# Kernel optimization log

Measured on AMD Instinct MI355X. Metric: run time of the kernel, lower is better.

Reference implementation:

```python
import jax, jax.numpy as jnp
import numpy as np

B, T, S, A = 4, 10, 6, 6
HID, L, IMG = 512, 6, 128
NCH = 16  # spatial-softmax channels
_px, _py = np.meshgrid(np.linspace(-1.0, 1.0, IMG), np.linspace(-1.0, 1.0, IMG))
POSX = jnp.asarray(_px.reshape(-1), jnp.float32)
POSY = jnp.asarray(_py.reshape(-1), jnp.float32)


def _conv_relu(x, w, b):
    y = jax.lax.conv_general_dilated(x, w, (1, 1), 'SAME',
                                     dimension_numbers=('NCHW', 'OIHW', 'NCHW'))
    return jax.nn.relu(y + b[None, :, None, None])


def _cnn_ss(x, ws, bs):
    for w, b in zip(ws, bs):
        x = _conv_relu(x, w, b)
    n = x.shape[0]
    attn = jax.nn.softmax(x.reshape(n, NCH, -1), axis=-1)  # (n, 16, H*W)
    ex = attn @ POSX  # (n, 16)
    ey = attn @ POSY
    return jnp.stack([ex, ey], axis=-1).reshape(n, 2 * NCH)  # (n, 32)


def _lstm_cell(x, h, c, wih, whh, bih, bhh):
    g = x @ wih.T + bih + h @ whh.T + bhh
    i, f, gg, o = jnp.split(g, 4, axis=-1)  # torch LSTMCell gate order i,f,g,o
    c2 = jax.nn.sigmoid(f) * c + jax.nn.sigmoid(i) * jnp.tanh(gg)
    h2 = jax.nn.sigmoid(o) * jnp.tanh(c2)
    return h2, c2


def setup_inputs() -> dict:
    key = jax.random.key(0)
    ks = iter(jax.random.split(key, 64))

    def nrm(shape, s=0.05):
        return jax.random.normal(next(ks), shape, dtype=jnp.float32) * s

    inp = {
        'seq_img_main': nrm((B, T, 3, IMG, IMG), 1.0),
        'seq_img_secondary': nrm((B, T, 3, IMG, IMG), 1.0),
        'seq_states': nrm((B, T, S), 1.0),
    }
    chans = [(32, 3), (64, 32), (128, 64), (16, 128)]
    for cam in ('m', 's'):
        for j, (o, ci) in enumerate(chans):
            inp[f'{cam}_w{j}'] = nrm((o, ci, 3, 3))
            inp[f'{cam}_b{j}'] = nrm((o,))
    in0, inr = S + 64, HID + 64  # 70 and 576
    inp['wih0'] = nrm((4 * HID, in0)); inp['whh0'] = nrm((4 * HID, HID))
    inp['bih0'] = nrm((4 * HID,)); inp['bhh0'] = nrm((4 * HID,))
    inp['wih_r'] = nrm((L - 1, 4 * HID, inr)); inp['whh_r'] = nrm((L - 1, 4 * HID, HID))
    inp['bih_r'] = nrm((L - 1, 4 * HID)); inp['bhh_r'] = nrm((L - 1, 4 * HID))
    inp['out_w'] = nrm((A, inr)); inp['out_b'] = nrm((A,))
    return inp


def reference(seq_img_main, seq_img_secondary, seq_states,
              m_w0, m_b0, m_w1, m_b1, m_w2, m_b2, m_w3, m_b3,
              s_w0, s_b0, s_w1, s_b1, s_w2, s_b2, s_w3, s_b3,
              wih0, whh0, bih0, bhh0, wih_r, whh_r, bih_r, bhh_r,
              out_w, out_b):
    b, t = seq_img_main.shape[:2]
    fm = _cnn_ss(seq_img_main.reshape(b * t, 3, IMG, IMG),
                 [m_w0, m_w1, m_w2, m_w3], [m_b0, m_b1, m_b2, m_b3])
    fs = _cnn_ss(seq_img_secondary.reshape(b * t, 3, IMG, IMG),
                 [s_w0, s_w1, s_w2, s_w3], [s_b0, s_b1, s_b2, s_b3])
    img = jnp.concatenate([fm, fs], axis=-1).reshape(b, t, 64)  # (B,T,64)

    h0 = jnp.zeros((L, b, HID), jnp.float32)
    c0 = jnp.zeros((L, b, HID), jnp.float32)

    def step(carry, xt):
        h, c = carry
        st, im = xt  # (B,S), (B,64)
        x = jnp.concatenate([st, im], axis=-1)
        hn, cn = _lstm_cell(x, h[0], c[0], wih0, whh0, bih0, bhh0)
        hs, cs = [hn], [cn]
        for l in range(L - 1):
            x = jnp.concatenate([hs[-1], im], axis=-1)
            hl, cl = _lstm_cell(x, h[l + 1], c[l + 1],
                                wih_r[l], whh_r[l], bih_r[l], bhh_r[l])
            hs.append(hl); cs.append(cl)
        out = jnp.concatenate([hs[-1], im], axis=-1) @ out_w.T + out_b
        return (jnp.stack(hs), jnp.stack(cs)), out

    _, outs = jax.lax.scan(step, (h0, c0),
                           (seq_states.transpose(1, 0, 2), img.transpose(1, 0, 2)))
    return outs.transpose(1, 0, 2)  # (B,T,A)
```

## Files before the change

### kernel.cpp

```cpp
#include <hip/hip_runtime.h>
#include <hip/hip_bf16.h>
#include <math.h>

typedef __hip_bfloat16 bf16;
typedef short bf16x8 __attribute__((ext_vector_type(8)));
typedef float f32x4 __attribute__((ext_vector_type(4)));

static constexpr int HWPX = 16384;

__device__ inline float sigmoidf_(float x) { return 1.0f / (1.0f + expf(-x)); }
__device__ inline float bflo(unsigned u) { return __uint_as_float(u << 16); }
__device__ inline float bfhi(unsigned u) { return __uint_as_float(u & 0xffff0000u); }
__device__ inline int swz(int x) { return (x ^ (x >> 2)) & 3; }

__device__ inline void gll16(const bf16* g, short* l) {
    __builtin_amdgcn_global_load_lds(
        (const __attribute__((address_space(1))) void*)g,
        (__attribute__((address_space(3))) void*)l, 16, 0, 0);
}

__global__ __launch_bounds__(256) void prep_lstm_k(
    const float* __restrict__ wih0, const float* __restrict__ whh0,
    const float* __restrict__ wihr, const float* __restrict__ whhr,
    bf16* __restrict__ d0, bf16* __restrict__ d1,
    bf16* __restrict__ d2, bf16* __restrict__ d3)
{
    const size_t nA = 2048ull * 72, nB = 2048ull * 512;
    const size_t nC = 5ull * 2048 * 576, nD = 5ull * 2048 * 512;
    for (size_t i = blockIdx.x * 256ull + threadIdx.x; i < nA + nB + nC + nD;
         i += (size_t)gridDim.x * 256) {
        if (i < nA) {
            int c = (int)(i % 72), r = (int)(i / 72);
            d0[i] = __float2bfloat16(c < 70 ? wih0[(size_t)r * 70 + c] : 0.f);
        } else if (i < nA + nB) {
            size_t k = i - nA; d1[k] = __float2bfloat16(whh0[k]);
        } else if (i < nA + nB + nC) {
            size_t k = i - nA - nB; d2[k] = __float2bfloat16(wihr[k]);
        } else {
            size_t k = i - nA - nB - nC; d3[k] = __float2bfloat16(whhr[k]);
        }
    }
}

struct ConvW {
    const float* src[8];
    bf16* dst[8];
};

__global__ __launch_bounds__(256) void prep_conv_k(ConvW a)
{
    const int sizes[4] = {3072, 18432, 73728, 18432};
    const int cins[4] = {3, 32, 64, 128};
    const int couts[4] = {32, 64, 128, 16};
    int total = 2 * 113664;
    for (int idx = blockIdx.x * 256 + threadIdx.x; idx < total; idx += gridDim.x * 256) {
        int i = idx, cam = 0;
        if (i >= 113664) { cam = 1; i -= 113664; }
        int layer = 0;
        while (layer < 3 && i >= sizes[layer]) { i -= sizes[layer]; ++layer; }
        const float* w = a.src[cam * 4 + layer];
        bf16* d = a.dst[cam * 4 + layer];
        if (layer == 0) {
            int k = i & 31, co = (i >> 5) & 31, ky = i >> 10;
            int kx = k >> 3, c = k & 7;
            float v = (kx < 3 && c < 3) ? w[((co * 3 + c) * 3 + ky) * 3 + kx] : 0.f;
            d[i] = __float2bfloat16(v);
        } else {
            int CIN = cins[layer], COUT = couts[layer], KC = CIN / 32;
            int e = i & 7;
            int t2 = i >> 3;
            int co = t2 % COUT;
            int t3 = t2 / COUT;
            int q = t3 & 3;
            int t4 = t3 >> 2;
            int kc = t4 % KC;
            int tap = t4 / KC;
            d[i] = __float2bfloat16(w[((size_t)(co * CIN + kc * 32 + q * 8 + e)) * 9 + tap]);
        }
    }
}

__global__ __launch_bounds__(256, 4) void conv01(
    const float* __restrict__ srcm, const float* __restrict__ srcs,
    const bf16* __restrict__ w0m, const bf16* __restrict__ w0s,
    const float* __restrict__ b0m, const float* __restrict__ b0s,
    const bf16* __restrict__ wTm, const bf16* __restrict__ wTs,
    const float* __restrict__ bm, const float* __restrict__ bs,
    bf16* __restrict__ out, int c0)
{
    constexpr int COUT = 64, MW = 2;
    constexpr int SLOTS = 4 * 264;

    const int y0 = (blockIdx.x >> 1) * 2;
    const int x0 = (blockIdx.x & 1) * 64;
    const int cam = blockIdx.y;
    const int img = blockIdx.z;
    const int ci_ = cam * gridDim.z + img;
    const float* inImg = (cam ? srcs : srcm) + (size_t)(c0 + img) * 3 * HWPX;
    const bf16* wT0 = cam ? w0s : w0m;
    const float* bias0 = cam ? b0s : b0m;
    const bf16* wT = cam ? wTs : wTm;
    const float* bias = cam ? bs : bm;
    const int tid = threadIdx.x;
    const int wave = tid >> 6, lane = tid & 63;
    const int wrow = wave >> 1, wm = wave & 1;
    const int q = lane >> 4, n16 = lane & 15;

    __shared__ short smem[SLOTS * 8];
    __shared__ short raw[6 * 68 * 16];

    for (int i = tid; i < SLOTS; i += 256)
        *(bf16x8*)(void*)&smem[i * 8] = (bf16x8)0;

    for (int d = tid; d < 6 * 68; d += 256) {
        int x = d % 68, r = d / 68;
        int yy = y0 - 2 + r, xx = x0 - 2 + x;
        bf16 v8[8];
#pragma unroll
        for (int c = 0; c < 8; ++c) v8[c] = __float2bfloat16(0.f);
        if ((unsigned)yy < 128u && (unsigned)xx < 128u) {
            int o = yy * 128 + xx;
            v8[0] = __float2bfloat16(inImg[o]);
            v8[1] = __float2bfloat16(inImg[HWPX + o]);
            v8[2] = __float2bfloat16(inImg[2 * HWPX + o]);
        }
        *(bf16x8*)(void*)&raw[d * 16] = *(bf16x8*)(void*)v8;
        *(bf16x8*)(void*)&raw[d * 16 + 8] = (bf16x8)0;
    }
    __syncthreads();

    const int co0_ = wm * 16 + n16;
    for (int rp = 0; rp < 4; ++rp) {
        int Y = y0 - 1 + rp;
        if ((unsigned)Y >= 128u) continue;
        for (int xg = wrow; xg < 5; xg += 2) {
            int xt = xg * 16 + n16;
            int xts = xt < 66 ? xt : 65;
            f32x4 a0 = f32x4{0.f, 0.f, 0.f, 0.f};
#pragma unroll
            for (int ky = 0; ky < 3; ++ky) {
                bf16x8 aF = *(const bf16x8*)(const void*)(wT0 +
                    ((size_t)(ky * 32 + co0_) * 32) + q * 8);
                int off = (q < 3) ? ((rp + ky) * 68 + xts + q) * 16
                                  : ((rp + ky) * 68 + xts) * 16 + 8;
                bf16x8 bF = *(const bf16x8*)(const void*)&raw[off];
                a0 = __builtin_amdgcn_mfma_f32_16x16x32_bf16(aF, bF, a0, 0, 0, 0);
            }
            int X = x0 - 1 + xt;
            if (xt < 66 && (unsigned)X < 128u) {
                int cb0 = wm * 16 + q * 4;
                bf16 tmp[4];
#pragma unroll
                for (int r = 0; r < 4; ++r) {
                    float v = a0[r] + bias0[cb0 + r];
                    tmp[r] = __float2bfloat16(v > 0.f ? v : 0.f);
                }
                int g = cb0 >> 3;
                int sbase = (rp * 264 + xt * 4 + (g ^ swz(xt))) * 8 + (q & 1) * 4;
                *reinterpret_cast<uint2*>(&smem[sbase]) = *reinterpret_cast<uint2*>(tmp);
            }
        }
    }
    __syncthreads();

    f32x4 acc[MW][4];
#pragma unroll
    for (int mt = 0; mt < MW; ++mt)
#pragma unroll
        for (int nt = 0; nt < 4; ++nt) acc[mt][nt] = f32x4{0.f, 0.f, 0.f, 0.f};

#pragma unroll
    for (int ky = 0; ky < 3; ++ky) {
#pragma unroll
        for (int kx = 0; kx < 3; ++kx) {
            bf16x8 aF[MW];
#pragma unroll
            for (int mt = 0; mt < MW; ++mt) {
                int co = (wm * MW + mt) * 16 + n16;
                aF[mt] = *(const bf16x8*)(const void*)(wT +
                    (((size_t)(ky * 3 + kx) * 4 + q) * COUT + co) * 8);
            }
#pragma unroll
            for (int nt = 0; nt < 4; ++nt) {
                int xt = nt * 16 + n16 + kx;
                int slot = (wrow + ky) * 264 + xt * 4 + (q ^ swz(xt));
                bf16x8 bF = *(const bf16x8*)(const void*)&smem[slot * 8];
#pragma unroll
                for (int mt = 0; mt < MW; ++mt)
                    acc[mt][nt] = __builtin_amdgcn_mfma_f32_16x16x32_bf16(
                        aF[mt], bF, acc[mt][nt], 0, 0, 0);
            }
        }
    }

    const int y = y0 + wrow;
#pragma unroll
    for (int mt = 0; mt < MW; ++mt) {
        int co0 = (wm * MW + mt) * 16 + q * 4;
#pragma unroll
        for (int nt = 0; nt < 4; ++nt) {
            int x = x0 + nt * 16 + n16;
            bf16 tmp[4];
#pragma unroll
            for (int r = 0; r < 4; ++r) {
                float v = acc[mt][nt][r] + bias[co0 + r];
                tmp[r] = __float2bfloat16(v > 0.f ? v : 0.f);
            }
            *reinterpret_cast<uint2*>(out + ((size_t)ci_ * HWPX + y * 128 + x) * COUT + co0)
                = *reinterpret_cast<uint2*>(tmp);
        }
    }
}

template <int CIN, int COUT>
__global__ __launch_bounds__(256, 4) void conv2r(
    const bf16* __restrict__ in, const bf16* __restrict__ wTm,
    const bf16* __restrict__ wTs, const float* __restrict__ bm,
    const float* __restrict__ bs, bf16* __restrict__ out,
    const char* __restrict__ zpage)
{
    constexpr int KC = CIN / 32;
    constexpr int NB = (KC > 1) ? 2 : 1;
    constexpr int MW = COUT / 32;
    constexpr int SLOTS = 4 * 264;

    const int y0 = (blockIdx.x >> 1) * 2;
    const int x0 = (blockIdx.x & 1) * 64;
    const int cam = blockIdx.y;
    const int img = blockIdx.z;
    const int ci_ = cam * gridDim.z + img;
    const bf16* wT = cam ? wTs : wTm;
    const float* bias = cam ? bs : bm;
    const int tid = threadIdx.x;
    const int wave = tid >> 6, lane = tid & 63;
    const int wrow = wave >> 1, wm = wave & 1;
    const int q = lane >> 4, n16 = lane & 15;

    __shared__ short smem[NB][SLOTS * 8];
    const bf16* inImg = in + (size_t)ci_ * HWPX * CIN;

    const bf16* sptr[5];
#pragma unroll
    for (int it = 0; it < 5; ++it) {
        int s = it * 256 + tid;
        int r = s / 264, s2 = s - r * 264;
        int sx = s2 >> 2;
        int g = (s2 & 3) ^ swz(sx);
        int yy = y0 + r - 1, xx = x0 + sx - 1;
        bool ok = (s < SLOTS) && ((unsigned)yy < 128u) && ((unsigned)xx < 128u);
        sptr[it] = ok ? inImg + ((size_t)yy * 128 + xx) * CIN + g * 8
                      : (const bf16*)(zpage + (tid & 255) * 16);
    }
    auto stage = [&](int kc, int buf) {
#pragma unroll
        for (int it = 0; it < 5; ++it) {
            if (it * 256 + tid < SLOTS)
                gll16(sptr[it] + kc * 32, &smem[buf][it * 2048 + wave * 512]);
        }
    };

    f32x4 acc[MW][4];
#pragma unroll
    for (int mt = 0; mt < MW; ++mt)
#pragma unroll
        for (int nt = 0; nt < 4; ++nt) acc[mt][nt] = f32x4{0.f, 0.f, 0.f, 0.f};

    stage(0, 0);
    for (int kc = 0; kc < KC; ++kc) {
        __syncthreads();
        if (kc + 1 < KC) stage(kc + 1, (kc + 1) % NB);
        const short* sb = smem[kc % NB];
#pragma unroll
        for (int ky = 0; ky < 3; ++ky) {
#pragma unroll
            for (int kx = 0; kx < 3; ++kx) {
                bf16x8 aF[MW];
#pragma unroll
                for (int mt = 0; mt < MW; ++mt) {
                    int co = (wm * MW + mt) * 16 + n16;
                    aF[mt] = *(const bf16x8*)(const void*)(wT +
                        ((((size_t)(ky * 3 + kx) * KC + kc) * 4 + q) * COUT + co) * 8);
                }
#pragma unroll
                for (int nt = 0; nt < 4; ++nt) {
                    int xt = nt * 16 + n16 + kx;
                    int slot = (wrow + ky) * 264 + xt * 4 + (q ^ swz(xt));
                    bf16x8 bF = *(const bf16x8*)(const void*)&sb[slot * 8];
#pragma unroll
                    for (int mt = 0; mt < MW; ++mt)
                        acc[mt][nt] = __builtin_amdgcn_mfma_f32_16x16x32_bf16(
                            aF[mt], bF, acc[mt][nt], 0, 0, 0);
                }
            }
        }
    }

    const int y = y0 + wrow;
#pragma unroll
    for (int mt = 0; mt < MW; ++mt) {
        int co0 = (wm * MW + mt) * 16 + q * 4;
#pragma unroll
        for (int nt = 0; nt < 4; ++nt) {
            int x = x0 + nt * 16 + n16;
            bf16 tmp[4];
#pragma unroll
            for (int r = 0; r < 4; ++r) {
                float v = acc[mt][nt][r] + bias[co0 + r];
                tmp[r] = __float2bfloat16(v > 0.f ? v : 0.f);
            }
            *reinterpret_cast<uint2*>(out + ((size_t)ci_ * HWPX + y * 128 + x) * COUT + co0)
                = *reinterpret_cast<uint2*>(tmp);
        }
    }
}

__global__ __launch_bounds__(256, 6) void conv4_xs(
    const bf16* __restrict__ in, const bf16* __restrict__ wTm,
    const bf16* __restrict__ wTs, const float* __restrict__ bm,
    const float* __restrict__ bs,
    float* __restrict__ partial,
    const char* __restrict__ zpage, int c0)
{
    constexpr int CIN = 128, COUT = 16, KC = 4;
    constexpr int SLOTS = 3 * 66 * 4;
    const int y = blockIdx.x >> 1;
    const int xh = blockIdx.x & 1;
    const int x0 = xh * 64;
    const int cam = blockIdx.y;
    const int img = blockIdx.z;
    const int ci_ = cam * gridDim.z + img;
    const int gimg = cam * 40 + c0 + img;
    const bf16* wT = cam ? wTs : wTm;
    const float* bias = cam ? bs : bm;
    const int tid = threadIdx.x;
    const int wave = tid >> 6, lane = tid & 63;
    const int q = lane >> 4, n16 = lane & 15;

    __shared__ short smem[2][SLOTS * 8];
    __shared__ float sred[3][4][16];
    const bf16* inImg = in + (size_t)ci_ * HWPX * CIN;

    const bf16* sptr[4];
#pragma unroll
    for (int it = 0; it < 4; ++it) {
        int s = it * 256 + tid;
        int r = s / 264, s2 = s - r * 264;
        int sx = s2 >> 2;
        int g = (s2 & 3) ^ swz(sx);
        int yy = y + r - 1, xx = x0 + sx - 1;
        bool ok = (s < SLOTS) && ((unsigned)yy < 128u) && ((unsigned)xx < 128u);
        sptr[it] = ok ? inImg + ((size_t)yy * 128 + xx) * CIN + g * 8
                      : (const bf16*)(zpage + (tid & 255) * 16);
    }
    auto stage = [&](int kc, int buf) {
#pragma unroll
        for (int it = 0; it < 4; ++it) {
            if (it * 256 + tid < SLOTS)
                gll16(sptr[it] + kc * 32, &smem[buf][it * 2048 + wave * 512]);
        }
    };

    f32x4 acc = f32x4{0.f, 0.f, 0.f, 0.f};

    stage(0, 0);
    for (int kc = 0; kc < KC; ++kc) {
        __syncthreads();
        if (kc + 1 < KC) stage(kc + 1, (kc + 1) & 1);
        const short* sb = smem[kc & 1];
#pragma unroll
        for (int ky = 0; ky < 3; ++ky) {
#pragma unroll
            for (int kx = 0; kx < 3; ++kx) {
                bf16x8 aF = *(const bf16x8*)(const void*)(wT +
                    ((((size_t)(ky * 3 + kx) * KC + kc) * 4 + q) * COUT + n16) * 8);
                int xt = wave * 16 + n16 + kx;
                int slot = xt * 4 + (q ^ swz(xt));
                bf16x8 bF = *(const bf16x8*)(const void*)&sb[ky * 2112 + slot * 8];
                acc = __builtin_amdgcn_mfma_f32_16x16x32_bf16(aF, bF, acc, 0, 0, 0);
            }
        }
    }

    float v[4];
    int x = x0 + wave * 16 + n16;
    float px = -1.f + (2.f / 127.f) * x;
#pragma unroll
    for (int r = 0; r < 4; ++r) {
        float t = acc[r] + bias[q * 4 + r];
        v[r] = t > 0.f ? t : 0.f;
    }
    float M[4];
#pragma unroll
    for (int r = 0; r < 4; ++r) {
        M[r] = v[r];
        M[r] = fmaxf(M[r], __shfl_xor(M[r], 1));
        M[r] = fmaxf(M[r], __shfl_xor(M[r], 2));
        M[r] = fmaxf(M[r], __shfl_xor(M[r], 4));
        M[r] = fmaxf(M[r], __shfl_xor(M[r], 8));
    }
    if (n16 == 0)
#pragma unroll
        for (int r = 0; r < 4; ++r) sred[0][wave][q * 4 + r] = M[r];
    __syncthreads();
#pragma unroll
    for (int r = 0; r < 4; ++r) {
        M[r] = fmaxf(fmaxf(sred[0][0][q * 4 + r], sred[0][1][q * 4 + r]),
                     fmaxf(sred[0][2][q * 4 + r], sred[0][3][q * 4 + r]));
    }
    float s[4], sx[4];
#pragma unroll
    for (int r = 0; r < 4; ++r) {
        float e = expf(v[r] - M[r]);
        s[r] = e; sx[r] = e * px;
        s[r] += __shfl_xor(s[r], 1);  sx[r] += __shfl_xor(sx[r], 1);
        s[r] += __shfl_xor(s[r], 2);  sx[r] += __shfl_xor(sx[r], 2);
        s[r] += __shfl_xor(s[r], 4);  sx[r] += __shfl_xor(sx[r], 4);
        s[r] += __shfl_xor(s[r], 8);  sx[r] += __shfl_xor(sx[r], 8);
    }
    __syncthreads();
    if (n16 == 0)
#pragma unroll
        for (int r = 0; r < 4; ++r) {
            sred[1][wave][q * 4 + r] = s[r];
            sred[2][wave][q * 4 + r] = sx[r];
        }
    __syncthreads();
    if (tid < 16) {
        float S = sred[1][0][tid] + sred[1][1][tid] + sred[1][2][tid] + sred[1][3][tid];
        float SX = sred[2][0][tid] + sred[2][1][tid] + sred[2][2][tid] + sred[2][3][tid];
        float Mv = fmaxf(fmaxf(sred[0][0][tid], sred[0][1][tid]),
                         fmaxf(sred[0][2][tid], sred[0][3][tid]));
        float* pp = partial + (((size_t)gimg * 16 + tid) * 256 + (y * 2 + xh)) * 4;
        pp[0] = Mv; pp[1] = S; pp[2] = SX;
    }
}

__global__ __launch_bounds__(256) void ssmerge_k(
    const float* __restrict__ partial, float* __restrict__ featm,
    float* __restrict__ feats)
{
    const int img = blockIdx.x;
    const int cam = img / 40, li = img % 40;
    float* feat = cam ? feats : featm;
    const int tid = threadIdx.x;
    const int co = tid >> 4, s = tid & 15;
    const float* base = partial + ((size_t)img * 16 + co) * 256 * 4;
    float M = -1e30f, S = 0.f, SX = 0.f, SY = 0.f;
    for (int i = s; i < 256; i += 16) {
        float m = base[i * 4], sv = base[i * 4 + 1], sxv = base[i * 4 + 2];
        float py = -1.f + (2.f / 127.f) * (i >> 1);
        float Mn = fmaxf(M, m);
        float w0 = expf(M - Mn), w1 = expf(m - Mn);
        S = S * w0 + sv * w1;
        SX = SX * w0 + sxv * w1;
        SY = SY * w0 + sv * py * w1;
        M = Mn;
    }
#pragma unroll
    for (int mask = 1; mask < 16; mask <<= 1) {
        float Mo = __shfl_xor(M, mask), So = __shfl_xor(S, mask);
        float SXo = __shfl_xor(SX, mask), SYo = __shfl_xor(SY, mask);
        float Mn = fmaxf(M, Mo);
        float w0 = expf(M - Mn), w1 = expf(Mo - Mn);
        S = S * w0 + So * w1; SX = SX * w0 + SXo * w1; SY = SY * w0 + SYo * w1;
        M = Mn;
    }
    if (s == 0) {
        feat[(size_t)li * 32 + 2 * co] = SX / S;
        feat[(size_t)li * 32 + 2 * co + 1] = SY / S;
    }
}

__device__ inline float imgfeat(const float* featm, const float* feats,
                                int b, int t, int k)
{
    int idx = (b * 10 + t) * 32;
    return k < 32 ? featm[idx + k] : feats[idx + k - 32];
}

template <int NB1>
__device__ inline void cell_mm(const bf16* __restrict__ wih,
                               const bf16* __restrict__ whh,
                               const float* __restrict__ xs0,
                               int j, int sub, float (&dg)[4][4])
{
    constexpr int K1 = NB1 * 8;
    constexpr int XS = K1 + 512;
#pragma unroll
    for (int r = 0; r < 4; ++r) {
        const uint4* __restrict__ w1 =
            reinterpret_cast<const uint4*>(wih + (size_t)(j + r * 512) * K1);
#pragma unroll
        for (int g0 = 0; g0 < NB1; g0 += 8) {
            int g = g0 + sub;
            if (g0 + 7 < NB1 || g < NB1) {
                uint4 u = w1[g];
                float a0 = bflo(u.x), a1 = bfhi(u.x), a2 = bflo(u.y), a3 = bfhi(u.y);
                float a4 = bflo(u.z), a5 = bfhi(u.z), a6 = bflo(u.w), a7 = bfhi(u.w);
#pragma unroll
                for (int b = 0; b < 4; ++b) {
                    const float* xp = xs0 + b * XS + g * 8;
                    dg[r][b] += a0 * xp[0] + a1 * xp[1] + a2 * xp[2] + a3 * xp[3]
                              + a4 * xp[4] + a5 * xp[5] + a6 * xp[6] + a7 * xp[7];
                }
            }
        }
        const uint4* __restrict__ w2 =
            reinterpret_cast<const uint4*>(whh + (size_t)(j + r * 512) * 512);
#pragma unroll
        for (int gi = 0; gi < 8; ++gi) {
            int g = gi * 8 + sub;
            uint4 u = w2[g];
            float a0 = bflo(u.x), a1 = bfhi(u.x), a2 = bflo(u.y), a3 = bfhi(u.y);
            float a4 = bflo(u.z), a5 = bfhi(u.z), a6 = bflo(u.w), a7 = bfhi(u.w);
#pragma unroll
            for (int b = 0; b < 4; ++b) {
                const float* xp = xs0 + b * XS + K1 + g * 8;
                dg[r][b] += a0 * xp[0] + a1 * xp[1] + a2 * xp[2] + a3 * xp[3]
                          + a4 * xp[4] + a5 * xp[5] + a6 * xp[6] + a7 * xp[7];
            }
        }
    }
}

template <int NB1>
__device__ inline void cell_step(
    int l, int t, int bx,
    const bf16* __restrict__ wih, const bf16* __restrict__ whh,
    const float* __restrict__ bih, const float* __restrict__ bhh,
    const float* __restrict__ states,
    const float* __restrict__ featm, const float* __restrict__ feats,
    float* __restrict__ hAll, float* __restrict__ cst,
    float* __restrict__ xs)
{
    constexpr int K1 = NB1 * 8;
    constexpr int XS = K1 + 512;
    const int tid = threadIdx.x;
    const int jloc = tid >> 3;
    const int sub = tid & 7;
    const int j = bx * 32 + jloc;

    const float* hprev = (l == 0) ? nullptr
                       : hAll + ((size_t)(t + 1) * 6 + (l - 1)) * 2048;
    const float* hold  = hAll + ((size_t)t * 6 + l) * 2048;
    float* hnew        = hAll + ((size_t)(t + 1) * 6 + l) * 2048;

    if (NB1 == 72) {
        for (int i = tid; i < 4 * 512; i += 256) {
            int bb = i >> 9, kk = i & 511;
            float2 cv;
            int base;
            if (kk < 256) {
                cv = *reinterpret_cast<const float2*>(&hprev[bb * 512 + kk * 2]);
                base = bb * XS + kk * 2;
            } else {
                cv = *reinterpret_cast<const float2*>(&hold[bb * 512 + (kk - 256) * 2]);
                base = bb * XS + 576 + (kk - 256) * 2;
            }
            xs[base] = cv.x; xs[base + 1] = cv.y;
        }
        {
            int bb = tid >> 6, k = tid & 63;
            xs[bb * XS + 512 + k] = imgfeat(featm, feats, bb, t, k);
        }
    } else {
        for (int i = tid; i < 4 * 256; i += 256) {
            int bb = i >> 8, kk = i & 255;
            float2 cv = *reinterpret_cast<const float2*>(&hold[bb * 512 + kk * 2]);
            int base = bb * XS + 72 + kk * 2;
            xs[base] = cv.x; xs[base + 1] = cv.y;
        }
        for (int i = tid; i < 4 * 72; i += 256) {
            int bb = i / 72, k = i - bb * 72;
            float v = (k < 6) ? states[(bb * 10 + t) * 6 + k]
                              : (k < 70 ? imgfeat(featm, feats, bb, t, k - 6) : 0.f);
            xs[bb * XS + k] = v;
        }
    }
    __syncthreads();

    float dg[4][4] = {{0.f, 0.f, 0.f, 0.f}, {0.f, 0.f, 0.f, 0.f},
                      {0.f, 0.f, 0.f, 0.f}, {0.f, 0.f, 0.f, 0.f}};
    cell_mm<NB1>(wih, whh, xs, j, sub, dg);

#pragma unroll
    for (int r = 0; r < 4; ++r)
#pragma unroll
        for (int b = 0; b < 4; ++b) {
            dg[r][b] += __shfl_xor(dg[r][b], 1);
            dg[r][b] += __shfl_xor(dg[r][b], 2);
            dg[r][b] += __shfl_xor(dg[r][b], 4);
        }

    if (sub == 0) {
        float b0 = bih[j] + bhh[j];
        float b1 = bih[j + 512] + bhh[j + 512];
        float b2 = bih[j + 1024] + bhh[j + 1024];
        float b3 = bih[j + 1536] + bhh[j + 1536];
#pragma unroll
        for (int b = 0; b < 4; ++b) {
            float gi = dg[0][b] + b0;
            float gf = dg[1][b] + b1;
            float gg = dg[2][b] + b2;
            float go = dg[3][b] + b3;
            float cp = cst[b * 512 + j];
            float c2 = sigmoidf_(gf) * cp + sigmoidf_(gi) * tanhf(gg);
            float h2 = sigmoidf_(go) * tanhf(c2);
            cst[b * 512 + j] = c2;
            hnew[b * 512 + j] = h2;
        }
    }
}

__global__ __launch_bounds__(256) void lstm_diag2_k(
    const bf16* __restrict__ wih0p, const bf16* __restrict__ whh0b,
    const bf16* __restrict__ wihrb, const bf16* __restrict__ whhrb,
    const float* __restrict__ bih0, const float* __restrict__ bhh0,
    const float* __restrict__ bihr, const float* __restrict__ bhhr,
    const float* __restrict__ states,
    const float* __restrict__ featm, const float* __restrict__ feats,
    float* __restrict__ hAll, float* __restrict__ cAll,
    const float* __restrict__ out_w, const float* __restrict__ out_b,
    float* __restrict__ out, int d)
{
    const int l = blockIdx.y;
    const int bx = blockIdx.x;
    const int tid = threadIdx.x;
    __shared__ float xs[4 * 1088];

    if (l == 6) {
        int t = d - 6;
        if (t < 0 || t >= 10 || bx != 0) return;
        const float* h5 = hAll + ((size_t)(t + 1) * 6 + 5) * 2048;
        int p = tid >> 3, sub = tid & 7;
        if (p >= 24) return;
        int b = p / 6, a = p % 6;
        const float* wr = out_w + a * 576;
        float acc = 0.f;
        for (int k = sub; k < 256; k += 8) {
            float2 cv = *reinterpret_cast<const float2*>(&h5[b * 512 + k * 2]);
            acc += wr[k * 2] * cv.x + wr[k * 2 + 1] * cv.y;
        }
        for (int k = sub; k < 64; k += 8)
            acc += wr[512 + k] * imgfeat(featm, feats, b, t, k);
        acc += __shfl_xor(acc, 1);
        acc += __shfl_xor(acc, 2);
        acc += __shfl_xor(acc, 4);
        if (sub == 0) out[(b * 10 + t) * 6 + a] = acc + out_b[a];
        return;
    }

    const int t = d - l;
    if (t < 0 || t >= 10) return;

    float* cst = cAll + (size_t)l * 2048;
    if (l == 0) {
        cell_step<9>(0, t, bx, wih0p, whh0b, bih0, bhh0,
                     states, featm, feats, hAll, cst, xs);
    } else {
        const bf16* wih = wihrb + (size_t)(l - 1) * 2048 * 576;
        const bf16* whh = whhrb + (size_t)(l - 1) * 2048 * 512;
        const float* bih = bihr + (l - 1) * 2048;
        const float* bhh = bhhr + (l - 1) * 2048;
        cell_step<72>(l, t, bx, wih, whh, bih, bhh,
                      states, featm, feats, hAll, cst, xs);
    }
}

extern "C" void kernel_launch(void* const* d_in, const int* in_sizes, int n_in,
                              void* d_out, int out_size, void* d_ws, size_t ws_size,
                              hipStream_t stream)
{
    const float* seq_m = (const float*)d_in[0];
    const float* seq_s = (const float*)d_in[1];
    const float* states = (const float*)d_in[2];
    const float *cw[2][4], *cb[2][4];
    for (int cam = 0; cam < 2; ++cam)
        for (int j = 0; j < 4; ++j) {
            cw[cam][j] = (const float*)d_in[3 + cam * 8 + j * 2];
            cb[cam][j] = (const float*)d_in[3 + cam * 8 + j * 2 + 1];
        }
    const float* wih0  = (const float*)d_in[19];
    const float* whh0  = (const float*)d_in[20];
    const float* bih0  = (const float*)d_in[21];
    const float* bhh0  = (const float*)d_in[22];
    const float* wih_r = (const float*)d_in[23];
    const float* whh_r = (const float*)d_in[24];
    const float* bih_r = (const float*)d_in[25];
    const float* bhh_r = (const float*)d_in[26];
    const float* out_w = (const float*)d_in[27];
    const float* out_b = (const float*)d_in[28];
    float* out = (float*)d_out;

    char* wsc = (char*)d_ws;
    auto carve = [&](size_t bytes) {
        char* p = wsc;
        wsc += (bytes + 255) & ~(size_t)255;
        return p;
    };
    float* featm = (float*)carve(40 * 32 * 4);
    float* feats = (float*)carve(40 * 32 * 4);
    float* hAll  = (float*)carve((size_t)11 * 6 * 2048 * 4);
    float* cAll  = (float*)carve((size_t)6 * 2048 * 4);
    char*  zpage = carve(8192);
    float* partial = (float*)carve((size_t)80 * 16 * 256 * 4 * 4);
    const int wtElts[4] = {3072, 18432, 73728, 18432};
    bf16* wT[2][4];
    for (int cam = 0; cam < 2; ++cam)
        for (int j = 0; j < 4; ++j) wT[cam][j] = (bf16*)carve(wtElts[j] * 2);
    bf16* wih0p = (bf16*)carve((size_t)2048 * 72 * 2);
    bf16* whh0b = (bf16*)carve((size_t)2048 * 512 * 2);
    bf16* wihrb = (bf16*)carve((size_t)5 * 2048 * 576 * 2);
    bf16* whhrb = (bf16*)carve((size_t)5 * 2048 * 512 * 2);

    size_t used = (size_t)(wsc - (char*)d_ws);
    size_t rem = ws_size > used ? ws_size - used : 0;
    int CHI = 1;
    const int cands[8] = {40, 20, 10, 8, 5, 4, 2, 1};
    for (int i = 0; i < 8; ++i) {
        size_t need = (size_t)2 * cands[i] * (128 + 64) * HWPX * 2;
        if (need <= rem) { CHI = cands[i]; break; }
    }
    bf16* bufA = (bf16*)carve((size_t)2 * CHI * HWPX * 128 * 2);
    bf16* bufB = (bf16*)carve((size_t)2 * CHI * HWPX * 64 * 2);

    hipMemsetAsync(hAll, 0, 6 * 2048 * 4, stream);
    hipMemsetAsync(cAll, 0, 6 * 2048 * 4, stream);
    hipMemsetAsync(zpage, 0, 8192, stream);

    prep_lstm_k<<<2048, 256, 0, stream>>>(wih0, whh0, wih_r, whh_r,
                                          wih0p, whh0b, wihrb, whhrb);
    ConvW cwArg;
    for (int cam = 0; cam < 2; ++cam)
        for (int j = 0; j < 4; ++j) {
            cwArg.src[cam * 4 + j] = cw[cam][j];
            cwArg.dst[cam * 4 + j] = wT[cam][j];
        }
    prep_conv_k<<<888, 256, 0, stream>>>(cwArg);

    for (int c0 = 0; c0 < 40; c0 += CHI) {
        int ch = (40 - c0) < CHI ? (40 - c0) : CHI;
        conv01<<<dim3(128, 2, ch), 256, 0, stream>>>(
            seq_m, seq_s, wT[0][0], wT[1][0], cb[0][0], cb[1][0],
            wT[0][1], wT[1][1], cb[0][1], cb[1][1], bufB, c0);
        conv2r<64, 128><<<dim3(128, 2, ch), 256, 0, stream>>>(
            bufB, wT[0][2], wT[1][2], cb[0][2], cb[1][2], bufA, zpage);
        conv4_xs<<<dim3(256, 2, ch), 256, 0, stream>>>(
            bufA, wT[0][3], wT[1][3], cb[0][3], cb[1][3], partial, zpage, c0);
    }
    ssmerge_k<<<80, 256, 0, stream>>>(partial, featm, feats);

    for (int d = 0; d < 16; ++d) {
        lstm_diag2_k<<<dim3(16, 7), 256, 0, stream>>>(
            wih0p, whh0b, wihrb, whhrb, bih0, bhh0, bih_r, bhh_r,
            states, featm, feats, hAll, cAll, out_w, out_b, out, d);
    }
}
```

Before: 1.132 ms.

## Compute four output rows per block in final conv to reuse halo rows and weights

The last conv layer (128->16 channels with spatial-softmax partials) now processes four output rows per block instead of one. It stages six input rows in LDS for four rows of output, which cuts the 3x halo re-read down to 1.5x. Each weight fragment load is also reused across four MFMAs. The cost is more LDS per block, more accumulator registers and a lower occupancy hint (launch bounds 2 instead of 6), and the grid has a quarter as many blocks.

Result: no change. 1.113 ms (-1.6%).

```diff
diff --git a/kernel.cpp b/kernel.cpp
--- a/kernel.cpp
+++ b/kernel.cpp
@@ -314,16 +314,17 @@
     }
 }
 
-__global__ __launch_bounds__(256, 6) void conv4_xs(
+__global__ __launch_bounds__(256, 2) void conv4_r4(
     const bf16* __restrict__ in, const bf16* __restrict__ wTm,
     const bf16* __restrict__ wTs, const float* __restrict__ bm,
     const float* __restrict__ bs,
     float* __restrict__ partial,
     const char* __restrict__ zpage, int c0)
 {
-    constexpr int CIN = 128, COUT = 16, KC = 4;
-    constexpr int SLOTS = 3 * 66 * 4;
-    const int y = blockIdx.x >> 1;
+    constexpr int CIN = 128, KC = 4;
+    constexpr int RR = 4;
+    constexpr int SLOTS = (RR + 2) * 264;
+    const int y0 = (blockIdx.x >> 1) * RR;
     const int xh = blockIdx.x & 1;
     const int x0 = xh * 64;
     const int cam = blockIdx.y;
@@ -337,30 +338,32 @@
     const int q = lane >> 4, n16 = lane & 15;
 
     __shared__ short smem[2][SLOTS * 8];
-    __shared__ float sred[3][4][16];
+    __shared__ float sred[3][RR][4][16];
     const bf16* inImg = in + (size_t)ci_ * HWPX * CIN;
 
-    const bf16* sptr[4];
-#pragma unroll
-    for (int it = 0; it < 4; ++it) {
+    const bf16* sptr[7];
+#pragma unroll
+    for (int it = 0; it < 7; ++it) {
         int s = it * 256 + tid;
         int r = s / 264, s2 = s - r * 264;
         int sx = s2 >> 2;
         int g = (s2 & 3) ^ swz(sx);
-        int yy = y + r - 1, xx = x0 + sx - 1;
+        int yy = y0 + r - 1, xx = x0 + sx - 1;
         bool ok = (s < SLOTS) && ((unsigned)yy < 128u) && ((unsigned)xx < 128u);
         sptr[it] = ok ? inImg + ((size_t)yy * 128 + xx) * CIN + g * 8
                       : (const bf16*)(zpage + (tid & 255) * 16);
     }
     auto stage = [&](int kc, int buf) {
 #pragma unroll
-        for (int it = 0; it < 4; ++it) {
+        for (int it = 0; it < 7; ++it) {
             if (it * 256 + tid < SLOTS)
                 gll16(sptr[it] + kc * 32, &smem[buf][it * 2048 + wave * 512]);
         }
     };
 
-    f32x4 acc = f32x4{0.f, 0.f, 0.f, 0.f};
+    f32x4 acc[RR];
+#pragma unroll
+    for (int rp = 0; rp < RR; ++rp) acc[rp] = f32x4{0.f, 0.f, 0.f, 0.f};
 
     stage(0, 0);
     for (int kc = 0; kc < KC; ++kc) {
@@ -372,65 +375,82 @@
 #pragma unroll
             for (int kx = 0; kx < 3; ++kx) {
                 bf16x8 aF = *(const bf16x8*)(const void*)(wT +
-                    ((((size_t)(ky * 3 + kx) * KC + kc) * 4 + q) * COUT + n16) * 8);
+                    ((((size_t)(ky * 3 + kx) * KC + kc) * 4 + q) * 16 + n16) * 8);
                 int xt = wave * 16 + n16 + kx;
-                int slot = xt * 4 + (q ^ swz(xt));
-                bf16x8 bF = *(const bf16x8*)(const void*)&sb[ky * 2112 + slot * 8];
-                acc = __builtin_amdgcn_mfma_f32_16x16x32_bf16(aF, bF, acc, 0, 0, 0);
-            }
-        }
-    }
-
-    float v[4];
+                int sbase = xt * 4 + (q ^ swz(xt));
+#pragma unroll
+                for (int rp = 0; rp < RR; ++rp) {
+                    bf16x8 bF = *(const bf16x8*)(const void*)
+                        &sb[((rp + ky) * 264 + sbase) * 8];
+                    acc[rp] = __builtin_amdgcn_mfma_f32_16x16x32_bf16(
+                        aF, bF, acc[rp], 0, 0, 0);
+                }
+            }
+        }
+    }
+
     int x = x0 + wave * 16 + n16;
     float px = -1.f + (2.f / 127.f) * x;
-#pragma unroll
-    for (int r = 0; r < 4; ++r) {
-        float t = acc[r] + bias[q * 4 + r];
-        v[r] = t > 0.f ? t : 0.f;
-    }
-    float M[4];
-#pragma unroll
-    for (int r = 0; r < 4; ++r) {
-        M[r] = v[r];
-        M[r] = fmaxf(M[r], __shfl_xor(M[r], 1));
-        M[r] = fmaxf(M[r], __shfl_xor(M[r], 2));
-        M[r] = fmaxf(M[r], __shfl_xor(M[r], 4));
-        M[r] = fmaxf(M[r], __shfl_xor(M[r], 8));
-    }
+    float v[RR][4], M[RR][4];
+#pragma unroll
+    for (int rp = 0; rp < RR; ++rp)
+#pragma unroll
+        for (int r = 0; r < 4; ++r) {
+            float t = acc[rp][r] + bias[q * 4 + r];
+            v[rp][r] = t > 0.f ? t : 0.f;
+            M[rp][r] = v[rp][r];
+        }
+#pragma unroll
+    for (int rp = 0; rp < RR; ++rp)
+#pragma unroll
+        for (int r = 0; r < 4; ++r) {
+            M[rp][r] = fmaxf(M[rp][r], __shfl_xor(M[rp][r], 1));
+            M[rp][r] = fmaxf(M[rp][r], __shfl_xor(M[rp][r], 2));
+            M[rp][r] = fmaxf(M[rp][r], __shfl_xor(M[rp][r], 4));
+            M[rp][r] = fmaxf(M[rp][r], __shfl_xor(M[rp][r], 8));
+        }
     if (n16 == 0)
 #pragma unroll
-        for (int r = 0; r < 4; ++r) sred[0][wave][q * 4 + r] = M[r];
+        for (int rp = 0; rp < RR; ++rp)
+#pragma unroll
+            for (int r = 0; r < 4; ++r) sred[0][rp][wave][q * 4 + r] = M[rp][r];
     __syncthreads();
 #pragma unroll
-    for (int r = 0; r < 4; ++r) {
-        M[r] = fmaxf(fmaxf(sred[0][0][q * 4 + r], sred[0][1][q * 4 + r]),
-                     fmaxf(sred[0][2][q * 4 + r], sred[0][3][q * 4 + r]));
-    }
-    float s[4], sx[4];
-#pragma unroll
-    for (int r = 0; r < 4; ++r) {
-        float e = expf(v[r] - M[r]);
-        s[r] = e; sx[r] = e * px;
-        s[r] += __shfl_xor(s[r], 1);  sx[r] += __shfl_xor(sx[r], 1);
-        s[r] += __shfl_xor(s[r], 2);  sx[r] += __shfl_xor(sx[r], 2);
-        s[r] += __shfl_xor(s[r], 4);  sx[r] += __shfl_xor(sx[r], 4);
-        s[r] += __shfl_xor(s[r], 8);  sx[r] += __shfl_xor(sx[r], 8);
-    }
+    for (int rp = 0; rp < RR; ++rp)
+#pragma unroll
+        for (int r = 0; r < 4; ++r) {
+            M[rp][r] = fmaxf(fmaxf(sred[0][rp][0][q * 4 + r], sred[0][rp][1][q * 4 + r]),
+                             fmaxf(sred[0][rp][2][q * 4 + r], sred[0][rp][3][q * 4 + r]));
+        }
+    float s[RR][4], sx[RR][4];
+#pragma unroll
+    for (int rp = 0; rp < RR; ++rp)
+#pragma unroll
+        for (int r = 0; r < 4; ++r) {
+            float e = expf(v[rp][r] - M[rp][r]);
+            s[rp][r] = e; sx[rp][r] = e * px;
+            s[rp][r] += __shfl_xor(s[rp][r], 1);  sx[rp][r] += __shfl_xor(sx[rp][r], 1);
+            s[rp][r] += __shfl_xor(s[rp][r], 2);  sx[rp][r] += __shfl_xor(sx[rp][r], 2);
+            s[rp][r] += __shfl_xor(s[rp][r], 4);  sx[rp][r] += __shfl_xor(sx[rp][r], 4);
+            s[rp][r] += __shfl_xor(s[rp][r], 8);  sx[rp][r] += __shfl_xor(sx[rp][r], 8);
+        }
     __syncthreads();
     if (n16 == 0)
 #pragma unroll
-        for (int r = 0; r < 4; ++r) {
-            sred[1][wave][q * 4 + r] = s[r];
-            sred[2][wave][q * 4 + r] = sx[r];
-        }
+        for (int rp = 0; rp < RR; ++rp)
+#pragma unroll
+            for (int r = 0; r < 4; ++r) {
+                sred[1][rp][wave][q * 4 + r] = s[rp][r];
+                sred[2][rp][wave][q * 4 + r] = sx[rp][r];
+            }
     __syncthreads();
-    if (tid < 16) {
-        float S = sred[1][0][tid] + sred[1][1][tid] + sred[1][2][tid] + sred[1][3][tid];
-        float SX = sred[2][0][tid] + sred[2][1][tid] + sred[2][2][tid] + sred[2][3][tid];
-        float Mv = fmaxf(fmaxf(sred[0][0][tid], sred[0][1][tid]),
-                         fmaxf(sred[0][2][tid], sred[0][3][tid]));
-        float* pp = partial + (((size_t)gimg * 16 + tid) * 256 + (y * 2 + xh)) * 4;
+    if (tid < 16 * RR) {
+        int rp = tid >> 4, c = tid & 15;
+        float S = sred[1][rp][0][c] + sred[1][rp][1][c] + sred[1][rp][2][c] + sred[1][rp][3][c];
+        float SX = sred[2][rp][0][c] + sred[2][rp][1][c] + sred[2][rp][2][c] + sred[2][rp][3][c];
+        float Mv = fmaxf(fmaxf(sred[0][rp][0][c], sred[0][rp][1][c]),
+                         fmaxf(sred[0][rp][2][c], sred[0][rp][3][c]));
+        float* pp = partial + (((size_t)gimg * 16 + c) * 256 + ((y0 + rp) * 2 + xh)) * 4;
         pp[0] = Mv; pp[1] = S; pp[2] = SX;
     }
 }
@@ -745,7 +765,7 @@
             wT[0][1], wT[1][1], cb[0][1], cb[1][1], bufB, c0);
         conv2r<64, 128><<<dim3(128, 2, ch), 256, 0, stream>>>(
             bufB, wT[0][2], wT[1][2], cb[0][2], cb[1][2], bufA, zpage);
-        conv4_xs<<<dim3(256, 2, ch), 256, 0, stream>>>(
+        conv4_r4<<<dim3(64, 2, ch), 256, 0, stream>>>(
             bufA, wT[0][3], wT[1][3], cb[0][3], cb[1][3], partial, zpage, c0);
     }
     ssmerge_k<<<80, 256, 0, stream>>>(partial, featm, feats);
```
